# Kernel optimization log

Hardware: AMD Instinct MI355X
Metric: run time of the kernel (lower is better)

Reference implementation:

```python
import jax, jax.numpy as jnp
import numpy as np

B, T, S, D, H = 2, 2048, 2048, 2048, 16
HD = D // H  # 128
SCALE = 1.0 / np.sqrt(HD)


def _rope(x, cos, sin):
    # x: [B,H,S,HD]; cos/sin: [1,1,S,HD//2]
    b, h, s, d = x.shape
    xs = x.reshape(b, h, s, d // 2, 2)
    x0, x1 = xs[..., 0], xs[..., 1]
    rot = jnp.stack([x0 * cos - x1 * sin, x1 * cos + x0 * sin], axis=-1)
    return rot.reshape(b, h, s, d)


def _split_heads(x):
    b, s, _ = x.shape
    return x.reshape(b, s, H, HD).transpose(0, 2, 1, 3)


def setup_inputs() -> dict:
    key = jax.random.key(0)
    ks = jax.random.split(key, 6)
    w_std = (1.0 / np.sqrt(2.0)) * np.sqrt(6.0 / (D + D))  # xavier_uniform with gain 1/sqrt(2)
    def xavier(k):
        return jax.random.uniform(k, (D, D), jnp.float32, -w_std, w_std)
    # rotary tables (standard inv-freq form)
    inv_freq = 1.0 / (10000.0 ** (np.arange(0, HD, 2, dtype=np.float32) / HD))  # [HD//2]
    ang = np.arange(T, dtype=np.float32)[:, None] * inv_freq[None, :]           # [T,HD//2]
    cos = jnp.asarray(np.cos(ang), jnp.float32)[None, None]  # [1,1,T,HD//2]
    sin = jnp.asarray(np.sin(ang), jnp.float32)[None, None]
    return {
        "hidden_states": jax.random.normal(ks[0], (B, T, D), jnp.float32),
        "encoder_hidden_states": jax.random.normal(ks[1], (B, S, D), jnp.float32),
        "Wq": xavier(ks[2]),
        "Wk": xavier(ks[3]),
        "Wv": xavier(ks[4]),
        "Wo": xavier(ks[5]),
        "cos_q": cos, "sin_q": sin,
        "cos_k": cos, "sin_k": sin,
    }


def reference(hidden_states, encoder_hidden_states, Wq, Wk, Wv, Wo,
              cos_q, sin_q, cos_k, sin_k):
    # Linear (no bias): y = x @ W.T
    q = _split_heads(jnp.einsum('btd,ed->bte', hidden_states, Wq))          # [B,H,T,HD]
    k = _split_heads(jnp.einsum('bsd,ed->bse', encoder_hidden_states, Wk))  # [B,H,S,HD]
    v = _split_heads(jnp.einsum('bsd,ed->bse', encoder_hidden_states, Wv))  # [B,H,S,HD]
    q = _rope(q, cos_q, sin_q)
    k = _rope(k, cos_k, sin_k)
    scores = jnp.einsum('bhtd,bhsd->bhts', q, k) * SCALE                    # [B,H,T,S]
    attn = jax.nn.softmax(scores.astype(jnp.float32), axis=-1)
    ctx = jnp.einsum('bhts,bhsd->bhtd', attn, v)                            # [B,H,T,HD]
    ctx = ctx.transpose(0, 2, 1, 3).reshape(B, T, D)                        # merge heads
    return jnp.einsum('btd,ed->bte', ctx, Wo)
```

## Files before the change

### kernel.cpp

```cpp
#include <hip/hip_runtime.h>
#include <cmath>

#define SCALE_F 0.088388347648318447f

typedef _Float16 f16;
typedef _Float16 f16x8 __attribute__((ext_vector_type(8)));
typedef _Float16 f16x4 __attribute__((ext_vector_type(4)));
typedef __fp16 fp16x2 __attribute__((ext_vector_type(2)));
typedef float f32x4 __attribute__((ext_vector_type(4)));
typedef float f32x16 __attribute__((ext_vector_type(16)));
typedef unsigned int u32;
typedef unsigned int u32x2 __attribute__((ext_vector_type(2)));
typedef unsigned int u32x4 __attribute__((ext_vector_type(4)));

#define MFMA16(a, b, c) __builtin_amdgcn_mfma_f32_16x16x32_f16(a, b, c, 0, 0, 0)
#define MFMA32(a, b, c) __builtin_amdgcn_mfma_f32_32x32x16_f16(a, b, c, 0, 0, 0)
#define Z16 ((f32x16){0.f,0.f,0.f,0.f,0.f,0.f,0.f,0.f,0.f,0.f,0.f,0.f,0.f,0.f,0.f,0.f})
#define EX2(x) __builtin_amdgcn_exp2f(x)

__device__ __forceinline__ void gl2lds16(const f16* g, f16* l) {
    __builtin_amdgcn_global_load_lds(
        (const __attribute__((address_space(1))) unsigned int*)g,
        (__attribute__((address_space(3))) unsigned int*)l, 16, 0, 0);
}

__device__ __forceinline__ u32 pkz(float x, float y) {
    fp16x2 h = __builtin_amdgcn_cvt_pkrtz(x, y);
    return __builtin_bit_cast(u32, h);
}
__device__ __forceinline__ float fswapsum(float x) {
    u32 a = __builtin_bit_cast(u32, x), b;
    asm volatile("v_mov_b32 %0, %1" : "=&v"(b) : "v"(a));
    asm volatile("v_permlane32_swap_b32 %0, %1" : "+v"(a), "+v"(b));
    return __builtin_bit_cast(float, a) + __builtin_bit_cast(float, b);
}
__device__ __forceinline__ float fswapmax(float x) {
    u32 a = __builtin_bit_cast(u32, x), b;
    asm volatile("v_mov_b32 %0, %1" : "=&v"(b) : "v"(a));
    asm volatile("v_permlane32_swap_b32 %0, %1" : "+v"(a), "+v"(b));
    return fmaxf(__builtin_bit_cast(float, a), __builtin_bit_cast(float, b));
}
#define MAX3(a, b, c) fmaxf(fmaxf((a), (b)), (c))

__global__ __launch_bounds__(256) void cvt_all(
    const float* __restrict__ hs, const float* __restrict__ es,
    const float* __restrict__ Wq, const float* __restrict__ Wk,
    const float* __restrict__ Wv, const float* __restrict__ Wo,
    f16* __restrict__ dst)
{
    const int c = blockIdx.x * 256 + threadIdx.x;
    const float* src; int off;
    if (c < 2097152) { src = (c < 1048576) ? hs : es; off = c & 1048575; }
    else {
        const int cc = c - 2097152;
        const int wsel = cc >> 19; off = cc & 524287;
        src = wsel == 0 ? Wq : wsel == 1 ? Wk : wsel == 2 ? Wv : Wo;
    }
    const float4* p = (const float4*)src + (size_t)off * 2;
    const float4 a = p[0], b2 = p[1];
    f16x8 o = {(f16)a.x, (f16)a.y, (f16)a.z, (f16)a.w,
               (f16)b2.x, (f16)b2.y, (f16)b2.z, (f16)b2.w};
    *(f16x8*)(dst + (size_t)c * 8) = o;
}

template <int OUT_MODE>
__global__ __launch_bounds__(256, 2) void gemm16(
    const f16* __restrict__ A, const f16* __restrict__ W,
    void* __restrict__ Cv, int M, int N, int K,
    const float* __restrict__ Cs, const float* __restrict__ Sn)
{
    __shared__ __align__(16) f16 Al[128 * 64];
    __shared__ __align__(16) f16 Bl[128 * 64];
    const int tid = threadIdx.x;
    const int l = tid & 63, w = tid >> 6;
    const int wr = w >> 1, wc = w & 1;

    const int nwg = gridDim.x, cpx = nwg >> 3;
    const int bid = blockIdx.x;
    const int swz = (bid & 7) * cpx + (bid >> 3);
    const int nbn = N >> 7;
    const int bm = (swz / nbn) * 128, bn = (swz % nbn) * 128;

    f32x4 acc[4][4];
#pragma unroll
    for (int i = 0; i < 4; ++i)
#pragma unroll
        for (int j = 0; j < 4; ++j) acc[i][j] = (f32x4){0.f, 0.f, 0.f, 0.f};

    const int srow = tid >> 3;
    const int sg = tid & 7;

    for (int k0 = 0; k0 < K; k0 += 64) {
        __syncthreads();
#pragma unroll
        for (int i = 0; i < 4; ++i) {
            const int row = i * 32 + srow;
            const int lg = sg ^ (row & 7);
            gl2lds16(A + (size_t)(bm + row) * K + k0 + lg * 8, Al + row * 64 + sg * 8);
            gl2lds16(W + (size_t)(bn + row) * K + k0 + lg * 8, Bl + row * 64 + sg * 8);
        }
        __syncthreads();
#pragma unroll
        for (int kk = 0; kk < 2; ++kk) {
            f16x8 a[4], b[4];
            const int g = kk * 4 + (l >> 4);
#pragma unroll
            for (int m = 0; m < 4; ++m) {
                const int row = wr * 64 + m * 16 + (l & 15);
                a[m] = *(const f16x8*)(Al + row * 64 + (g ^ (row & 7)) * 8);
            }
#pragma unroll
            for (int n = 0; n < 4; ++n) {
                const int row = wc * 64 + n * 16 + (l & 15);
                b[n] = *(const f16x8*)(Bl + row * 64 + (g ^ (row & 7)) * 8);
            }
#pragma unroll
            for (int m = 0; m < 4; ++m)
#pragma unroll
                for (int n = 0; n < 4; ++n)
                    acc[m][n] = MFMA16(a[m], b[n], acc[m][n]);
        }
    }

#pragma unroll
    for (int m = 0; m < 4; ++m)
#pragma unroll
        for (int n = 0; n < 4; ++n)
#pragma unroll
            for (int j = 0; j < 4; ++j) {
                const int r = bm + wr * 64 + m * 16 + ((l >> 4) << 2) + j;
                const int c = bn + wc * 64 + n * 16 + (l & 15);
                if (OUT_MODE == 0) {
                    ((f16*)Cv)[(size_t)r * N + c] = (f16)acc[m][n][j];
                } else if (OUT_MODE == 2) {
                    ((float*)Cv)[(size_t)r * N + c] = acc[m][n][j];
                } else if (OUT_MODE == 3) {
                    ((f16*)Cv)[(size_t)((c >> 11) * 2048 + r) * 2048 + (c & 2047)] = (f16)acc[m][n][j];
                } else if (OUT_MODE == 4) {
                    const float v = acc[m][n][j];
                    const float vp = __shfl_xor(v, 1);
                    const int t = r & 2047;
                    const int i2 = (c & 127) >> 1;
                    const float co = Cs[t * 64 + i2];
                    const float si = Sn[t * 64 + i2];
                    const float y = (c & 1) ? fmaf(v, co, vp * si) : fmaf(v, co, -vp * si);
                    ((f16*)Cv)[(size_t)r * N + c] = (f16)y;
                }
            }
}

__global__ __launch_bounds__(256, 2) void attn16(
    const f16* __restrict__ Qg, const f16* __restrict__ Kg,
    const f16* __restrict__ Vt, f16* __restrict__ Og)
{
    __shared__ __align__(16) f16 Kl[64 * 132];
    __shared__ __align__(16) f16 Vl[128 * 68];
    __shared__ float bnc[4][32];

    const int tid = threadIdx.x;
    const int l = tid & 63, w = tid >> 6;
    const int l31 = l & 31, hi = l >> 5;
    const int hi4 = hi * 4;

    const int krow = tid >> 4, kg = tid & 15;
    const int vd = tid >> 3, vg = tid & 7;

    const int bid = blockIdx.x;
    const int swz = (bid & 7) * 64 + (bid >> 3);
    const int bh = swz >> 4, qt = swz & 15;
    const int b = bh >> 4, h = bh & 15;

    const int qrow = b * 2048 + qt * 128 + w * 32 + l31;
    const f16 qsc = (f16)(0.088388347648318447f * 1.44269504088896f);
    f16x8 qf[8];
#pragma unroll
    for (int kc = 0; kc < 8; ++kc) {
        f16x8 t0 = *(const f16x8*)(Qg + (size_t)qrow * 2048 + h * 128 + kc * 16 + hi * 8);
#pragma unroll
        for (int e = 0; e < 8; ++e) t0[e] = t0[e] * qsc;
        qf[kc] = t0;
    }

    f32x16 o[4] = {Z16, Z16, Z16, Z16};
    float mrow = -3.0e38f, lrow = 0.0f;

    const f16* Kbase = Kg + (size_t)(b * 2048) * 2048 + h * 128;
    const f16* Vbase = Vt + (size_t)(b * 2048 + h * 128) * 2048;

    u32x4 kst[4], vst[4];

#define LOADT(st) do {                                                                   \
    _Pragma("unroll")                                                                    \
    for (int u = 0; u < 4; ++u)                                                          \
        kst[u] = *(const u32x4*)(Kbase + (size_t)((st) + krow + u * 16) * 2048 + kg * 8);\
    _Pragma("unroll")                                                                    \
    for (int u = 0; u < 4; ++u)                                                          \
        vst[u] = *(const u32x4*)(Vbase + (size_t)(vd + u * 32) * 2048 + (st) + vg * 8);  \
} while (0)

#define WRITET() do {                                                                    \
    _Pragma("unroll")                                                                    \
    for (int u = 0; u < 4; ++u) {                                                        \
        f16* p = &Kl[(krow + u * 16) * 132 + kg * 8];                                    \
        *(u32x2*)p       = (u32x2){kst[u].x, kst[u].y};                                  \
        *(u32x2*)(p + 4) = (u32x2){kst[u].z, kst[u].w};                                  \
    }                                                                                    \
    _Pragma("unroll")                                                                    \
    for (int u = 0; u < 4; ++u) {                                                        \
        f16* p = &Vl[(vd + u * 32) * 68 + vg * 8];                                       \
        *(u32x2*)p       = (u32x2){vst[u].x, vst[u].y};                                  \
        *(u32x2*)(p + 4) = (u32x2){vst[u].z, vst[u].w};                                  \
    }                                                                                    \
} while (0)

    LOADT(0);
    WRITET();
    __syncthreads();

    for (int t = 0; t < 32; ++t) {
        if (t < 31) LOADT((t + 1) * 64);

        f32x16 p0 = Z16, p1 = Z16;
        __builtin_amdgcn_s_setprio(1);
#pragma unroll
        for (int kc = 0; kc < 8; ++kc) {
            const int go = (kc * 2 + hi) * 8;
            const f16* kp0 = Kl + l31 * 132 + go;
            const f16* kp1 = Kl + (32 + l31) * 132 + go;
            const f16x4 a0 = *(const f16x4*)kp0, a1 = *(const f16x4*)(kp0 + 4);
            const f16x4 b0 = *(const f16x4*)kp1, b1 = *(const f16x4*)(kp1 + 4);
            const f16x8 k0 = __builtin_shufflevector(a0, a1, 0, 1, 2, 3, 4, 5, 6, 7);
            const f16x8 k1 = __builtin_shufflevector(b0, b1, 0, 1, 2, 3, 4, 5, 6, 7);
            p0 = MFMA32(k0, qf[kc], p0);
            p1 = MFMA32(k1, qf[kc], p1);
        }
        __builtin_amdgcn_s_setprio(0);

        float pp[32];
#pragma unroll
        for (int r = 0; r < 16; ++r) { pp[r] = p0[r]; pp[16 + r] = p1[r]; }
        float mv[11];
#pragma unroll
        for (int i = 0; i < 10; ++i) mv[i] = MAX3(pp[3 * i], pp[3 * i + 1], pp[3 * i + 2]);
        mv[10] = fmaxf(pp[30], pp[31]);
        const float n0 = MAX3(mv[0], mv[1], mv[2]);
        const float n1 = MAX3(mv[3], mv[4], mv[5]);
        const float n2 = MAX3(mv[6], mv[7], mv[8]);
        const float n3 = MAX3(mv[9], mv[10], n0);
        float mx = MAX3(n1, n2, n3);
        mx = fswapmax(mx);

        if (!__all(mx <= mrow + 8.0f)) {
            const float mn = fmaxf(mrow, mx);
            const float cr = EX2(mrow - mn);
            mrow = mn;
            lrow *= cr;
            if (hi == 0) bnc[w][l31] = cr;
#pragma unroll
            for (int r = 0; r < 16; ++r) {
                const float crr = bnc[w][(r & 3) + 8 * (r >> 2) + 4 * hi];
                o[0][r] *= crr; o[1][r] *= crr; o[2][r] *= crr; o[3][r] *= crr;
            }
        }

        float st16[16];
#pragma unroll
        for (int r = 0; r < 16; ++r) {
            p0[r] = EX2(p0[r] - mrow);
            p1[r] = EX2(p1[r] - mrow);
            st16[r] = p0[r] + p1[r];
        }
#pragma unroll
        for (int r = 0; r < 8; ++r) st16[r] += st16[r + 8];
#pragma unroll
        for (int r = 0; r < 4; ++r) st16[r] += st16[r + 4];
        lrow += fswapsum((st16[0] + st16[1]) + (st16[2] + st16[3]));

        f16x8 pf[4];
#pragma unroll
        for (int ksl = 0; ksl < 2; ++ksl) {
            u32x4 w0 = {pkz(p0[8*ksl+0], p0[8*ksl+1]), pkz(p0[8*ksl+2], p0[8*ksl+3]),
                        pkz(p0[8*ksl+4], p0[8*ksl+5]), pkz(p0[8*ksl+6], p0[8*ksl+7])};
            pf[ksl] = __builtin_bit_cast(f16x8, w0);
            u32x4 w1 = {pkz(p1[8*ksl+0], p1[8*ksl+1]), pkz(p1[8*ksl+2], p1[8*ksl+3]),
                        pkz(p1[8*ksl+4], p1[8*ksl+5]), pkz(p1[8*ksl+6], p1[8*ksl+7])};
            pf[2 + ksl] = __builtin_bit_cast(f16x8, w1);
        }

        __builtin_amdgcn_s_setprio(1);
#pragma unroll
        for (int dt = 0; dt < 4; ++dt) {
            const f16* vrow = Vl + (dt * 32 + l31) * 68;
#pragma unroll
            for (int ks = 0; ks < 4; ++ks) {
                const f16x4 vlo = *(const f16x4*)(vrow + ks * 16 + hi4);
                const f16x4 vhi = *(const f16x4*)(vrow + ks * 16 + hi4 + 8);
                const f16x8 vf = __builtin_shufflevector(vlo, vhi, 0, 1, 2, 3, 4, 5, 6, 7);
                o[dt] = MFMA32(pf[ks], vf, o[dt]);
            }
        }
        __builtin_amdgcn_s_setprio(0);

        __syncthreads();
        if (t < 31) {
            WRITET();
            __syncthreads();
        }
    }
#undef LOADT
#undef WRITET

    const float inv = 1.0f / lrow;
    if (hi == 0) bnc[w][l31] = inv;
#pragma unroll
    for (int r = 0; r < 16; ++r) {
        const int qq = (r & 3) + 8 * (r >> 2) + 4 * hi;
        const float ir = bnc[w][qq];
        const size_t row = (size_t)(b * 2048 + qt * 128 + w * 32 + qq);
#pragma unroll
        for (int dt = 0; dt < 4; ++dt)
            Og[row * 2048 + h * 128 + dt * 32 + l31] = (f16)(o[dt][r] * ir);
    }
}

extern "C" void kernel_launch(void* const* d_in, const int* in_sizes, int n_in,
                              void* d_out, int out_size, void* d_ws, size_t ws_size,
                              hipStream_t stream) {
    const float* hs = (const float*)d_in[0];
    const float* es = (const float*)d_in[1];
    const float* Wq = (const float*)d_in[2];
    const float* Wk = (const float*)d_in[3];
    const float* Wv = (const float*)d_in[4];
    const float* Wo = (const float*)d_in[5];
    const float* cq = (const float*)d_in[6];
    const float* sq = (const float*)d_in[7];
    const float* ck = (const float*)d_in[8];
    const float* sk = (const float*)d_in[9];
    float* out = (float*)d_out;

    f16* hs16 = (f16*)d_ws;
    f16* es16 = hs16 + 8388608;
    f16* Wq16 = es16 + 8388608;
    f16* Wk16 = Wq16 + 4194304;
    f16* Wv16 = Wk16 + 4194304;
    f16* Wo16 = Wv16 + 4194304;
    f16* Q16  = Wo16 + 4194304;
    f16* K16  = Q16 + 8388608;
    f16* Vt16 = K16 + 8388608;
    f16* ctx16 = hs16;

    const dim3 tB(256);
    cvt_all<<<dim3(16384), tB, 0, stream>>>(hs, es, Wq, Wk, Wv, Wo, hs16);

    gemm16<4><<<dim3(512), tB, 0, stream>>>(hs16, Wq16, Q16, 4096, 2048, 2048, cq, sq);
    gemm16<4><<<dim3(512), tB, 0, stream>>>(es16, Wk16, K16, 4096, 2048, 2048, ck, sk);
    gemm16<3><<<dim3(512), tB, 0, stream>>>(Wv16, es16, Vt16, 2048, 4096, 2048, nullptr, nullptr);

    attn16<<<dim3(512), tB, 0, stream>>>(Q16, K16, Vt16, ctx16);

    gemm16<2><<<dim3(512), tB, 0, stream>>>(ctx16, Wo16, out, 4096, 2048, 2048, nullptr, nullptr);
}
```

Baseline: 289.3 us.

## Split attention over key dimension into two halves with softmax merge kernel

Each attention block now processes half of the key/value sequence, doubling the grid, and writes a normalized partial output plus its row max and sum. A new merge kernel combines the two partials using log-sum-exp weights. This aims to raise parallelism and shorten per-block latency, at the cost of extra global traffic for partial outputs and an extra launch.

```diff
diff --git a/kernel.cpp b/kernel.cpp
--- a/kernel.cpp
+++ b/kernel.cpp
@@ -151,7 +151,8 @@
 
 __global__ __launch_bounds__(256, 2) void attn16(
     const f16* __restrict__ Qg, const f16* __restrict__ Kg,
-    const f16* __restrict__ Vt, f16* __restrict__ Og)
+    const f16* __restrict__ Vt, f16* __restrict__ O0, f16* __restrict__ O1,
+    float* __restrict__ mlb)
 {
     __shared__ __align__(16) f16 Kl[64 * 132];
     __shared__ __align__(16) f16 Vl[128 * 68];
@@ -166,9 +167,12 @@
     const int vd = tid >> 3, vg = tid & 7;
 
     const int bid = blockIdx.x;
-    const int swz = (bid & 7) * 64 + (bid >> 3);
-    const int bh = swz >> 4, qt = swz & 15;
+    const int swz = (bid & 7) * 128 + (bid >> 3);
+    const int bh = swz >> 5;
+    const int sh = (swz >> 4) & 1;
+    const int qt = swz & 15;
     const int b = bh >> 4, h = bh & 15;
+    const int sbase = sh << 10;
 
     const int qrow = b * 2048 + qt * 128 + w * 32 + l31;
     const f16 qsc = (f16)(0.088388347648318447f * 1.44269504088896f);
@@ -213,12 +217,12 @@
     }                                                                                    \
 } while (0)
 
-    LOADT(0);
+    LOADT(sbase);
     WRITET();
     __syncthreads();
 
-    for (int t = 0; t < 32; ++t) {
-        if (t < 31) LOADT((t + 1) * 64);
+    for (int t = 0; t < 16; ++t) {
+        if (t < 15) LOADT(sbase + (t + 1) * 64);
 
         f32x16 p0 = Z16, p1 = Z16;
         __builtin_amdgcn_s_setprio(1);
@@ -302,7 +306,7 @@
         __builtin_amdgcn_s_setprio(0);
 
         __syncthreads();
-        if (t < 31) {
+        if (t < 15) {
             WRITET();
             __syncthreads();
         }
@@ -310,8 +314,14 @@
 #undef LOADT
 #undef WRITET
 
+    f16* Op = sh ? O1 : O0;
     const float inv = 1.0f / lrow;
-    if (hi == 0) bnc[w][l31] = inv;
+    if (hi == 0) {
+        bnc[w][l31] = inv;
+        const int unit = (qrow << 4) | h;
+        mlb[sh * 131072 + unit] = mrow;
+        mlb[sh * 131072 + 65536 + unit] = lrow;
+    }
 #pragma unroll
     for (int r = 0; r < 16; ++r) {
         const int qq = (r & 3) + 8 * (r >> 2) + 4 * hi;
@@ -319,8 +329,33 @@
         const size_t row = (size_t)(b * 2048 + qt * 128 + w * 32 + qq);
 #pragma unroll
         for (int dt = 0; dt < 4; ++dt)
-            Og[row * 2048 + h * 128 + dt * 32 + l31] = (f16)(o[dt][r] * ir);
-    }
+            Op[row * 2048 + h * 128 + dt * 32 + l31] = (f16)(o[dt][r] * ir);
+    }
+}
+
+__global__ __launch_bounds__(256) void merge2(
+    const f16* __restrict__ O0, const f16* __restrict__ O1,
+    const float* __restrict__ mlb, f16* __restrict__ Og)
+{
+    const int i = blockIdx.x * 256 + threadIdx.x;
+    const int unit = i >> 4, c8 = i & 15;
+    const float m0 = mlb[unit];
+    const float l0 = mlb[65536 + unit];
+    const float m1 = mlb[131072 + unit];
+    const float l1 = mlb[196608 + unit];
+    const float m = fmaxf(m0, m1);
+    const float w0 = l0 * EX2(m0 - m);
+    const float w1 = l1 * EX2(m1 - m);
+    const float inv = 1.0f / (w0 + w1);
+    const float a0 = w0 * inv, a1 = w1 * inv;
+    const size_t off = (size_t)unit * 128 + c8 * 8;
+    const f16x8 x0 = *(const f16x8*)(O0 + off);
+    const f16x8 x1 = *(const f16x8*)(O1 + off);
+    f16x8 r;
+#pragma unroll
+    for (int e = 0; e < 8; ++e)
+        r[e] = (f16)(a0 * (float)x0[e] + a1 * (float)x1[e]);
+    *(f16x8*)(Og + off) = r;
 }
 
 extern "C" void kernel_launch(void* const* d_in, const int* in_sizes, int n_in,
@@ -347,7 +382,10 @@
     f16* Q16  = Wo16 + 4194304;
     f16* K16  = Q16 + 8388608;
     f16* Vt16 = K16 + 8388608;
-    f16* ctx16 = hs16;
+    f16* Op0   = hs16;
+    f16* Op1   = es16;
+    float* mlb = (float*)Wq16;
+    f16* ctx16 = Q16;
 
     const dim3 tB(256);
     cvt_all<<<dim3(16384), tB, 0, stream>>>(hs, es, Wq, Wk, Wv, Wo, hs16);
@@ -356,7 +394,8 @@
     gemm16<4><<<dim3(512), tB, 0, stream>>>(es16, Wk16, K16, 4096, 2048, 2048, ck, sk);
     gemm16<3><<<dim3(512), tB, 0, stream>>>(Wv16, es16, Vt16, 2048, 4096, 2048, nullptr, nullptr);
 
-    attn16<<<dim3(512), tB, 0, stream>>>(Q16, K16, Vt16, ctx16);
+    attn16<<<dim3(1024), tB, 0, stream>>>(Q16, K16, Vt16, Op0, Op1, mlb);
+    merge2<<<dim3(4096), tB, 0, stream>>>(Op0, Op1, mlb, ctx16);
 
     gemm16<2><<<dim3(512), tB, 0, stream>>>(ctx16, Wo16, out, 4096, 2048, 2048, nullptr, nullptr);
 }
```

Measured after the change: 299.0 us. 1.03x slower.

## Fuse Q/K/V projections into one 256x256-tile double-buffered GEMM launch

Applied to the files above, without the earlier changes.

Replaces three separate 128x128-tile GEMM launches for the Q, K and V projections with a single kernel of 384 blocks of 512 threads. Each block computes a 256x256 tile with double-buffered LDS staging through direct global-to-LDS loads, overlapping the next K-slice loads with the current MFMAs, and uses setprio around the MFMA bursts. The intent is to cut launch overhead, raise arithmetic intensity per byte loaded, and fill the GPU with one wave of blocks. The larger tile uses 128 KB of LDS and many accumulator registers, which may limit occupancy. The output GEMM becomes a non-templated fp32-only variant.

```diff
diff --git a/kernel.cpp b/kernel.cpp
--- a/kernel.cpp
+++ b/kernel.cpp
@@ -1,7 +1,5 @@
 #include <hip/hip_runtime.h>
 #include <cmath>
-
-#define SCALE_F 0.088388347648318447f
 
 typedef _Float16 f16;
 typedef _Float16 f16x8 __attribute__((ext_vector_type(8)));
@@ -63,11 +61,136 @@
     *(f16x8*)(dst + (size_t)c * 8) = o;
 }
 
-template <int OUT_MODE>
-__global__ __launch_bounds__(256, 2) void gemm16(
+__global__ __launch_bounds__(512, 2) void qkv256(
+    const f16* __restrict__ hs, const f16* __restrict__ es,
+    const f16* __restrict__ Wq, const f16* __restrict__ Wk, const f16* __restrict__ Wv,
+    f16* __restrict__ Qo, f16* __restrict__ Ko, f16* __restrict__ Vo,
+    const float* __restrict__ cq, const float* __restrict__ sq,
+    const float* __restrict__ ck, const float* __restrict__ sk)
+{
+    __shared__ __align__(16) f16 LA[2][2][128 * 64];
+    __shared__ __align__(16) f16 LB[2][2][128 * 64];
+
+    const int tid = threadIdx.x;
+    const int l = tid & 63, w = tid >> 6;
+    const int wr = w >> 2, wc = w & 3;
+    const int lr = l & 15, lk = l >> 4;
+
+    const int bid = blockIdx.x;
+    const int swz = (bid & 7) * 48 + (bid >> 3);
+    const int prob = swz >> 7;
+    const int t128 = swz & 127;
+
+    const f16* A; const f16* W; int bm, bn;
+    if (prob == 0)      { A = hs; W = Wq; bm = (t128 >> 3) * 256; bn = (t128 & 7) * 256; }
+    else if (prob == 1) { A = es; W = Wk; bm = (t128 >> 3) * 256; bn = (t128 & 7) * 256; }
+    else                { A = Wv; W = es; bm = (t128 >> 4) * 256; bn = (t128 & 15) * 256; }
+
+    const int srow0 = tid >> 3, sg = tid & 7;
+
+#define STAGEH(dst, src, r0, k0) do {                                                    \
+    _Pragma("unroll")                                                                    \
+    for (int u = 0; u < 2; ++u) {                                                        \
+        const int row = u * 64 + srow0;                                                  \
+        const int lg = sg ^ (row & 7);                                                   \
+        gl2lds16((src) + (size_t)((r0) + row) * 2048 + (k0) + lg * 8,                    \
+                 (dst) + row * 64 + sg * 8);                                             \
+    }                                                                                    \
+} while (0)
+
+    f32x4 acc[8][4];
+#pragma unroll
+    for (int m = 0; m < 8; ++m)
+#pragma unroll
+        for (int n = 0; n < 4; ++n) acc[m][n] = (f32x4){0.f, 0.f, 0.f, 0.f};
+
+    STAGEH(LA[0][0], A, bm, 0);
+    STAGEH(LA[0][1], A, bm + 128, 0);
+    STAGEH(LB[0][0], W, bn, 0);
+    STAGEH(LB[0][1], W, bn + 128, 0);
+
+    for (int j = 0; j < 32; ++j) {
+        const int cur = j & 1;
+        const int k1 = (j + 1) * 64;
+#pragma unroll
+        for (int q = 0; q < 4; ++q) {
+            if (j < 31) {
+                if (q == 0)      STAGEH(LA[cur ^ 1][0], A, bm, k1);
+                else if (q == 1) STAGEH(LA[cur ^ 1][1], A, bm + 128, k1);
+                else if (q == 2) STAGEH(LB[cur ^ 1][0], W, bn, k1);
+                else             STAGEH(LB[cur ^ 1][1], W, bn + 128, k1);
+            }
+            if (q == 0) {
+                if (j < 31) asm volatile("s_waitcnt vmcnt(2)" ::: "memory");
+                else        asm volatile("s_waitcnt vmcnt(0)" ::: "memory");
+                __builtin_amdgcn_s_barrier();
+                __builtin_amdgcn_sched_barrier(0);
+            }
+
+            const int qm = q >> 1, qn = q & 1;
+            f16x8 a[4][2], b[2][2];
+#pragma unroll
+            for (int m = 0; m < 4; ++m) {
+                const int row = qm * 64 + m * 16 + lr;
+#pragma unroll
+                for (int k = 0; k < 2; ++k) {
+                    const int dg = k * 4 + lk;
+                    a[m][k] = *(const f16x8*)(LA[cur][wr] + row * 64 + (dg ^ (row & 7)) * 8);
+                }
+            }
+#pragma unroll
+            for (int n = 0; n < 2; ++n) {
+                const int rb = wc * 64 + qn * 32 + n * 16 + lr;
+                const int hb = rb >> 7, rh = rb & 127;
+#pragma unroll
+                for (int k = 0; k < 2; ++k) {
+                    const int dg = k * 4 + lk;
+                    b[n][k] = *(const f16x8*)(LB[cur][hb] + rh * 64 + (dg ^ (rh & 7)) * 8);
+                }
+            }
+            __builtin_amdgcn_s_setprio(1);
+#pragma unroll
+            for (int m = 0; m < 4; ++m)
+#pragma unroll
+                for (int n = 0; n < 2; ++n) {
+                    acc[qm * 4 + m][qn * 2 + n] = MFMA16(a[m][0], b[n][0], acc[qm * 4 + m][qn * 2 + n]);
+                    acc[qm * 4 + m][qn * 2 + n] = MFMA16(a[m][1], b[n][1], acc[qm * 4 + m][qn * 2 + n]);
+                }
+            __builtin_amdgcn_s_setprio(0);
+            __builtin_amdgcn_s_barrier();
+        }
+    }
+#undef STAGEH
+
+    const float* Cs = prob == 0 ? cq : ck;
+    const float* Sn = prob == 0 ? sq : sk;
+    f16* Out = prob == 0 ? Qo : Ko;
+#pragma unroll
+    for (int m = 0; m < 8; ++m)
+#pragma unroll
+        for (int n = 0; n < 4; ++n)
+#pragma unroll
+            for (int jj = 0; jj < 4; ++jj) {
+                const int r = bm + wr * 128 + m * 16 + (lk << 2) + jj;
+                const int c = bn + wc * 64 + n * 16 + lr;
+                const float v = acc[m][n][jj];
+                if (prob == 2) {
+                    Vo[(size_t)((c >> 11) * 2048 + r) * 2048 + (c & 2047)] = (f16)v;
+                } else {
+                    const float vp = __shfl_xor(v, 1);
+                    const int tt = r & 2047;
+                    const int i2 = (c & 127) >> 1;
+                    const float co = Cs[tt * 64 + i2];
+                    const float si = Sn[tt * 64 + i2];
+                    const float y = (c & 1) ? fmaf(v, co, vp * si) : fmaf(v, co, -vp * si);
+                    Out[(size_t)r * 2048 + c] = (f16)y;
+                }
+            }
+}
+
+__global__ __launch_bounds__(256, 2) void gemm16f(
     const f16* __restrict__ A, const f16* __restrict__ W,
-    void* __restrict__ Cv, int M, int N, int K,
-    const float* __restrict__ Cs, const float* __restrict__ Sn)
+    float* __restrict__ C, int M, int N, int K)
 {
     __shared__ __align__(16) f16 Al[128 * 64];
     __shared__ __align__(16) f16 Bl[128 * 64];
@@ -130,22 +253,7 @@
             for (int j = 0; j < 4; ++j) {
                 const int r = bm + wr * 64 + m * 16 + ((l >> 4) << 2) + j;
                 const int c = bn + wc * 64 + n * 16 + (l & 15);
-                if (OUT_MODE == 0) {
-                    ((f16*)Cv)[(size_t)r * N + c] = (f16)acc[m][n][j];
-                } else if (OUT_MODE == 2) {
-                    ((float*)Cv)[(size_t)r * N + c] = acc[m][n][j];
-                } else if (OUT_MODE == 3) {
-                    ((f16*)Cv)[(size_t)((c >> 11) * 2048 + r) * 2048 + (c & 2047)] = (f16)acc[m][n][j];
-                } else if (OUT_MODE == 4) {
-                    const float v = acc[m][n][j];
-                    const float vp = __shfl_xor(v, 1);
-                    const int t = r & 2047;
-                    const int i2 = (c & 127) >> 1;
-                    const float co = Cs[t * 64 + i2];
-                    const float si = Sn[t * 64 + i2];
-                    const float y = (c & 1) ? fmaf(v, co, vp * si) : fmaf(v, co, -vp * si);
-                    ((f16*)Cv)[(size_t)r * N + c] = (f16)y;
-                }
+                C[(size_t)r * N + c] = acc[m][n][j];
             }
 }
 
@@ -352,11 +460,10 @@
     const dim3 tB(256);
     cvt_all<<<dim3(16384), tB, 0, stream>>>(hs, es, Wq, Wk, Wv, Wo, hs16);
 
-    gemm16<4><<<dim3(512), tB, 0, stream>>>(hs16, Wq16, Q16, 4096, 2048, 2048, cq, sq);
-    gemm16<4><<<dim3(512), tB, 0, stream>>>(es16, Wk16, K16, 4096, 2048, 2048, ck, sk);
-    gemm16<3><<<dim3(512), tB, 0, stream>>>(Wv16, es16, Vt16, 2048, 4096, 2048, nullptr, nullptr);
+    qkv256<<<dim3(384), dim3(512), 0, stream>>>(hs16, es16, Wq16, Wk16, Wv16,
+                                                Q16, K16, Vt16, cq, sq, ck, sk);
 
     attn16<<<dim3(512), tB, 0, stream>>>(Q16, K16, Vt16, ctx16);
 
-    gemm16<2><<<dim3(512), tB, 0, stream>>>(ctx16, Wo16, out, 4096, 2048, 2048, nullptr, nullptr);
-}
+    gemm16f<<<dim3(512), tB, 0, stream>>>(ctx16, Wo16, out, 4096, 2048, 2048);
+}
```

Measured after the change: 390.5 us. 34.9% more time.
